# Kernel tuning notes

Measured on AMD Instinct MI355X. Metric: run time of the kernel, lower is better.

## Reference

```python
import jax, jax.numpy as jnp
import numpy as np

NUM_CLASSES = 12
C_SMOOTH = 5.0  # the `c` constant in compute_weights(distances, 5)


def setup_inputs() -> dict:
    key = jax.random.key(0)
    k1, k2 = jax.random.split(key)
    features = jax.random.normal(k1, (128, 512, 32, 32), dtype=jnp.float32)
    labels = jax.random.randint(k2, (128,), 0, NUM_CLASSES)
    return {"features": features, "labels": labels}


def _prototype_generation(features, labels, num_classes):
    # features: [b, c, h, w]; labels: [b] int
    b = features.shape[0]
    flat = features.reshape(b, -1)  # [b, d], d = c*h*w
    sq = jnp.sum(flat * flat, axis=1)  # [b]
    d2 = sq[:, None] + sq[None, :] - 2.0 * (flat @ flat.T)  # [b, b]
    d2 = jnp.maximum(d2, 0.0)
    # grad-safe sqrt: diagonal (and identical pairs) get dist 0 with grad 0,
    # matching torch.norm's subgradient at 0
    pos = d2 > 0
    dist = jnp.where(pos, jnp.sqrt(jnp.where(pos, d2, 1.0)), 0.0)  # [b, b]
    # sum of distances to same-label samples (includes self, dist 0)
    same = (labels[:, None] == labels[None, :]).astype(flat.dtype)  # [b, b]
    dsum = jnp.sum(dist * same, axis=1)  # [b]
    # compute_weights(distance_sum, 5) = 1 / (sqrt(ds^2 + 25) + 1e-12)
    w = 1.0 / (jnp.sqrt(dsum * dsum + C_SMOOTH * C_SMOOTH) + 1e-12)
    w = w / (jnp.sum(w) + 1e-12)  # normalized sample weights [b]
    # label-grouped weighted scatter-sum -> [num_classes, c, h, w]
    weighted = features * w[:, None, None, None]
    return jax.ops.segment_sum(weighted, labels, num_segments=num_classes)


def reference(features, labels):
    return _prototype_generation(features, labels, NUM_CLASSES)
```

## Files before the change

### kernel.cpp

```cpp
#include <hip/hip_runtime.h>
#include <math.h>

#define D_FEAT 524288
#define NSAMP  128
#define NCLS   12
#define BK     256
#define KPB    2048
#define NB     256
#define D4     131072

typedef __bf16 bf16x8 __attribute__((ext_vector_type(8)));
typedef float  f32x16 __attribute__((ext_vector_type(16)));

__device__ __forceinline__ unsigned pack_bf16(float a, float b) {
  unsigned ua = __float_as_uint(a); ua += 0x7fffu + ((ua >> 16) & 1u);
  unsigned ub = __float_as_uint(b); ub += 0x7fffu + ((ub >> 16) & 1u);
  return (ua >> 16) | (ub & 0xffff0000u);
}

__global__ __launch_bounds__(512, 2) void gram_k(const float* __restrict__ f,
                                                 float* __restrict__ gram,
                                                 float* __restrict__ partial,
                                                 int atomic_mode) {
  __shared__ __align__(16) unsigned char lds[BK * NSAMP * 2];
  const int t    = threadIdx.x;
  const int b    = blockIdx.x;
  const int wave = t >> 6;
  const int lane = t & 63;
  const int sl   = lane & 31;
  const int hi   = lane >> 5;
  const int Ra   = (wave >> 2) * 64;
  const int Ca   = (wave & 3) * 32;
  const int kq   = lane;
  const size_t k0 = (size_t)b * KPB;

  f32x16 acc0, acc1;
#pragma unroll
  for (int i = 0; i < 16; ++i) { acc0[i] = 0.f; acc1[i] = 0.f; }

  const int wg      = kq >> 1;
  const int halfsel = kq & 1;

  float4 pf[16];
#pragma unroll
  for (int i = 0; i < 16; ++i) {
    const int s = i * 8 + wave;
    pf[i] = *(const float4*)(f + (size_t)s * D_FEAT + k0 + kq * 4);
  }
#pragma unroll
  for (int i = 0; i < 16; ++i) {
    const int s = i * 8 + wave;
    uint2 p; p.x = pack_bf16(pf[i].x, pf[i].y); p.y = pack_bf16(pf[i].z, pf[i].w);
    *(uint2*)(lds + (size_t)(wg * NSAMP + (s ^ (wg & 7))) * 16 + halfsel * 8) = p;
  }

  for (int sli = 0; sli < KPB / BK; ++sli) {
    __syncthreads();
    if (sli < KPB / BK - 1) {
      const size_t kb = k0 + (size_t)(sli + 1) * BK;
#pragma unroll
      for (int i = 0; i < 16; ++i) {
        const int s = i * 8 + wave;
        pf[i] = *(const float4*)(f + (size_t)s * D_FEAT + kb + kq * 4);
      }
    }
#pragma unroll
    for (int t16 = 0; t16 < 16; ++t16) {
      const int g = 2 * t16 + hi, gx = g & 7;
      const unsigned char* base = lds + g * (NSAMP * 16);
      bf16x8 a0 = *(const bf16x8*)(base + (((Ra      + sl) ^ gx) << 4));
      bf16x8 a1 = *(const bf16x8*)(base + (((Ra + 32 + sl) ^ gx) << 4));
      bf16x8 b0 = *(const bf16x8*)(base + (((Ca      + sl) ^ gx) << 4));
      acc0 = __builtin_amdgcn_mfma_f32_32x32x16_bf16(a0, b0, acc0, 0, 0, 0);
      acc1 = __builtin_amdgcn_mfma_f32_32x32x16_bf16(a1, b0, acc1, 0, 0, 0);
    }
    __syncthreads();
    if (sli < KPB / BK - 1) {
#pragma unroll
      for (int i = 0; i < 16; ++i) {
        const int s = i * 8 + wave;
        uint2 p; p.x = pack_bf16(pf[i].x, pf[i].y); p.y = pack_bf16(pf[i].z, pf[i].w);
        *(uint2*)(lds + (size_t)(wg * NSAMP + (s ^ (wg & 7))) * 16 + halfsel * 8) = p;
      }
    }
  }

  if (atomic_mode) {
#pragma unroll
    for (int r = 0; r < 16; ++r) {
      const int row0 = Ra + 4 * hi + (r & 3) + 8 * (r >> 2);
      atomicAdd(gram + row0 * NSAMP + Ca + sl, acc0[r]);
      atomicAdd(gram + (row0 + 32) * NSAMP + Ca + sl, acc1[r]);
    }
  } else {
    float* p = partial + (size_t)b * (NSAMP * NSAMP);
#pragma unroll
    for (int r = 0; r < 16; ++r) {
      const int row0 = Ra + 4 * hi + (r & 3) + 8 * (r >> 2);
      p[row0 * NSAMP + Ca + sl]        = acc0[r];
      p[(row0 + 32) * NSAMP + Ca + sl] = acc1[r];
    }
  }
}

__global__ __launch_bounds__(256) void reduce_k(const float* __restrict__ partial,
                                                float* __restrict__ gram) {
  const int idx = blockIdx.x * 256 + threadIdx.x;
  float s = 0.f;
#pragma unroll 8
  for (int b = 0; b < NB; ++b) s += partial[(size_t)b * (NSAMP * NSAMP) + idx];
  gram[idx] = s;
}

__global__ void weights_k(const float* __restrict__ gram, const int* __restrict__ labels,
                          float* __restrict__ w_out, int* __restrict__ order_out,
                          int* __restrict__ off_out) {
  __shared__ float sq[NSAMP];
  __shared__ int   lab[NSAMP];
  __shared__ float wv[NSAMP];
  __shared__ float wsum_s;
  __shared__ int   cnt[NCLS];
  __shared__ int   off[NCLS + 1];
  const int t = threadIdx.x;
  lab[t] = labels[t];
  sq[t]  = gram[t * NSAMP + t];
  if (t < NCLS) cnt[t] = 0;
  __syncthreads();
  const int   myl = lab[t];
  const float st  = sq[t];
  float dsum = 0.f;
  for (int j = 0; j < NSAMP; ++j) {
    if (j != t && lab[j] == myl) {
      float d2 = st + sq[j] - 2.f * gram[t * NSAMP + j];
      if (d2 > 0.f) dsum += sqrtf(d2);
    }
  }
  const float wt = 1.f / (sqrtf(dsum * dsum + 25.f) + 1e-12f);
  wv[t] = wt;
  atomicAdd(&cnt[myl], 1);
  __syncthreads();
  if (t == 0) {
    float s = 0.f;
    for (int j = 0; j < NSAMP; ++j) s += wv[j];
    wsum_s = s;
    off[0] = 0;
    for (int c = 0; c < NCLS; ++c) off[c + 1] = off[c] + cnt[c];
  }
  __syncthreads();
  int rank = 0;
  for (int j = 0; j < t; ++j) rank += (lab[j] == myl) ? 1 : 0;
  const int pos  = off[myl] + rank;
  order_out[pos] = t;
  w_out[pos]     = wt / (wsum_s + 1e-12f);
  if (t <= NCLS) off_out[t] = off[t];
}

__global__ __launch_bounds__(256) void scatter_k(const float* __restrict__ f,
                                                 const float* __restrict__ w,
                                                 const int* __restrict__ order,
                                                 const int* __restrict__ off,
                                                 float* __restrict__ out) {
  __shared__ float w_l[NSAMP];
  __shared__ int   ord_l[NSAMP];
  __shared__ int   off_l[NCLS + 1];
  const int t = threadIdx.x;
  if (t < NSAMP) { w_l[t] = w[t]; ord_l[t] = order[t]; }
  if (t <= NCLS) off_l[t] = off[t];
  __syncthreads();
  const size_t d4 = (size_t)blockIdx.x * 256 + t;
  const float4* f4 = (const float4*)f;
  float4* o4 = (float4*)out;
  for (int c = 0; c < NCLS; ++c) {
    float4 acc = make_float4(0.f, 0.f, 0.f, 0.f);
    const int e = off_l[c + 1];
#pragma unroll 4
    for (int j = off_l[c]; j < e; ++j) {
      const float  wj = w_l[j];
      const float4 v  = f4[(size_t)ord_l[j] * D4 + d4];
      acc.x += wj * v.x; acc.y += wj * v.y; acc.z += wj * v.z; acc.w += wj * v.w;
    }
    o4[(size_t)c * D4 + d4] = acc;
  }
}

extern "C" void kernel_launch(void* const* d_in, const int* in_sizes, int n_in,
                              void* d_out, int out_size, void* d_ws, size_t ws_size,
                              hipStream_t stream) {
  const float* f      = (const float*)d_in[0];
  const int*   labels = (const int*)d_in[1];
  float* out  = (float*)d_out;
  float* ws_f = (float*)d_ws;

  float* gram     = ws_f;
  float* w_sorted = ws_f + 16384;
  int*   order    = (int*)(ws_f + 16384 + 128);
  int*   clsoff   = (int*)(ws_f + 16384 + 256);
  float* partial  = ws_f + 32768;

  const size_t need = (size_t)32768 * 4 + (size_t)NB * NSAMP * NSAMP * 4;
  const int atomic_mode = (ws_size < need) ? 1 : 0;

  if (atomic_mode) hipMemsetAsync(gram, 0, NSAMP * NSAMP * sizeof(float), stream);
  gram_k<<<NB, 512, 0, stream>>>(f, gram, partial, atomic_mode);
  if (!atomic_mode) reduce_k<<<64, 256, 0, stream>>>(partial, gram);
  weights_k<<<1, NSAMP, 0, stream>>>(gram, labels, w_sorted, order, clsoff);
  scatter_k<<<D4 / 256, 256, 0, stream>>>(f, w_sorted, order, clsoff, out);
}
```

Baseline: 480.7 us.

## Double gram blocks, split reduction across samples, and parallelize scatter over classes

The gram kernel now uses a half-size K slice per block (512 blocks, BK 128) with higher occupancy hints and a two-samples-per-wave load mapping. The partial reduction splits the block-sum across four thread groups with an LDS combine, giving 256 blocks instead of 64. The scatter kernel gets one block per class per chunk instead of looping over all classes in one block, which spreads the work over many more blocks. The costs are a partial buffer twice as large and more reduction traffic.

```diff
diff --git a/kernel.cpp b/kernel.cpp
--- a/kernel.cpp
+++ b/kernel.cpp
@@ -4,9 +4,9 @@
 #define D_FEAT 524288
 #define NSAMP  128
 #define NCLS   12
-#define BK     256
-#define KPB    2048
-#define NB     256
+#define BK     128
+#define KPB    1024
+#define NB     512
 #define D4     131072
 
 typedef __bf16 bf16x8 __attribute__((ext_vector_type(8)));
@@ -18,7 +18,7 @@
   return (ua >> 16) | (ub & 0xffff0000u);
 }
 
-__global__ __launch_bounds__(512, 2) void gram_k(const float* __restrict__ f,
+__global__ __launch_bounds__(512, 4) void gram_k(const float* __restrict__ f,
                                                  float* __restrict__ gram,
                                                  float* __restrict__ partial,
                                                  int atomic_mode) {
@@ -31,25 +31,25 @@
   const int hi   = lane >> 5;
   const int Ra   = (wave >> 2) * 64;
   const int Ca   = (wave & 3) * 32;
-  const int kq   = lane;
+  const int q    = lane & 31;
   const size_t k0 = (size_t)b * KPB;
 
   f32x16 acc0, acc1;
 #pragma unroll
   for (int i = 0; i < 16; ++i) { acc0[i] = 0.f; acc1[i] = 0.f; }
 
-  const int wg      = kq >> 1;
-  const int halfsel = kq & 1;
-
-  float4 pf[16];
-#pragma unroll
-  for (int i = 0; i < 16; ++i) {
-    const int s = i * 8 + wave;
-    pf[i] = *(const float4*)(f + (size_t)s * D_FEAT + k0 + kq * 4);
-  }
-#pragma unroll
-  for (int i = 0; i < 16; ++i) {
-    const int s = i * 8 + wave;
+  const int wg      = q >> 1;
+  const int halfsel = q & 1;
+
+  float4 pf[8];
+#pragma unroll
+  for (int i = 0; i < 8; ++i) {
+    const int s = i * 16 + wave * 2 + hi;
+    pf[i] = *(const float4*)(f + (size_t)s * D_FEAT + k0 + q * 4);
+  }
+#pragma unroll
+  for (int i = 0; i < 8; ++i) {
+    const int s = i * 16 + wave * 2 + hi;
     uint2 p; p.x = pack_bf16(pf[i].x, pf[i].y); p.y = pack_bf16(pf[i].z, pf[i].w);
     *(uint2*)(lds + (size_t)(wg * NSAMP + (s ^ (wg & 7))) * 16 + halfsel * 8) = p;
   }
@@ -59,14 +59,14 @@
     if (sli < KPB / BK - 1) {
       const size_t kb = k0 + (size_t)(sli + 1) * BK;
 #pragma unroll
-      for (int i = 0; i < 16; ++i) {
-        const int s = i * 8 + wave;
-        pf[i] = *(const float4*)(f + (size_t)s * D_FEAT + kb + kq * 4);
+      for (int i = 0; i < 8; ++i) {
+        const int s = i * 16 + wave * 2 + hi;
+        pf[i] = *(const float4*)(f + (size_t)s * D_FEAT + kb + q * 4);
       }
     }
 #pragma unroll
-    for (int t16 = 0; t16 < 16; ++t16) {
-      const int g = 2 * t16 + hi, gx = g & 7;
+    for (int step = 0; step < BK / 16; ++step) {
+      const int g = 2 * step + hi, gx = g & 7;
       const unsigned char* base = lds + g * (NSAMP * 16);
       bf16x8 a0 = *(const bf16x8*)(base + (((Ra      + sl) ^ gx) << 4));
       bf16x8 a1 = *(const bf16x8*)(base + (((Ra + 32 + sl) ^ gx) << 4));
@@ -77,8 +77,8 @@
     __syncthreads();
     if (sli < KPB / BK - 1) {
 #pragma unroll
-      for (int i = 0; i < 16; ++i) {
-        const int s = i * 8 + wave;
+      for (int i = 0; i < 8; ++i) {
+        const int s = i * 16 + wave * 2 + hi;
         uint2 p; p.x = pack_bf16(pf[i].x, pf[i].y); p.y = pack_bf16(pf[i].z, pf[i].w);
         *(uint2*)(lds + (size_t)(wg * NSAMP + (s ^ (wg & 7))) * 16 + halfsel * 8) = p;
       }
@@ -105,11 +105,17 @@
 
 __global__ __launch_bounds__(256) void reduce_k(const float* __restrict__ partial,
                                                 float* __restrict__ gram) {
-  const int idx = blockIdx.x * 256 + threadIdx.x;
+  __shared__ float red[256];
+  const int t  = threadIdx.x;
+  const int o  = blockIdx.x * 64 + (t & 63);
+  const int bs = t >> 6;
   float s = 0.f;
 #pragma unroll 8
-  for (int b = 0; b < NB; ++b) s += partial[(size_t)b * (NSAMP * NSAMP) + idx];
-  gram[idx] = s;
+  for (int b = bs * (NB / 4); b < (bs + 1) * (NB / 4); ++b)
+    s += partial[(size_t)b * (NSAMP * NSAMP) + o];
+  red[t] = s;
+  __syncthreads();
+  if (t < 64) gram[o] = red[t] + red[t + 64] + red[t + 128] + red[t + 192];
 }
 
 __global__ void weights_k(const float* __restrict__ gram, const int* __restrict__ labels,
@@ -162,25 +168,25 @@
                                                  float* __restrict__ out) {
   __shared__ float w_l[NSAMP];
   __shared__ int   ord_l[NSAMP];
-  __shared__ int   off_l[NCLS + 1];
-  const int t = threadIdx.x;
+  __shared__ int   jr[2];
+  const int t  = threadIdx.x;
+  const int c  = blockIdx.x >> 9;
+  const int cb = blockIdx.x & 511;
   if (t < NSAMP) { w_l[t] = w[t]; ord_l[t] = order[t]; }
-  if (t <= NCLS) off_l[t] = off[t];
-  __syncthreads();
-  const size_t d4 = (size_t)blockIdx.x * 256 + t;
+  if (t < 2) jr[t] = off[c + t];
+  __syncthreads();
+  const int j0 = jr[0], j1 = jr[1];
+  const size_t d4 = (size_t)cb * 256 + t;
   const float4* f4 = (const float4*)f;
   float4* o4 = (float4*)out;
-  for (int c = 0; c < NCLS; ++c) {
-    float4 acc = make_float4(0.f, 0.f, 0.f, 0.f);
-    const int e = off_l[c + 1];
+  float4 acc = make_float4(0.f, 0.f, 0.f, 0.f);
 #pragma unroll 4
-    for (int j = off_l[c]; j < e; ++j) {
-      const float  wj = w_l[j];
-      const float4 v  = f4[(size_t)ord_l[j] * D4 + d4];
-      acc.x += wj * v.x; acc.y += wj * v.y; acc.z += wj * v.z; acc.w += wj * v.w;
-    }
-    o4[(size_t)c * D4 + d4] = acc;
-  }
+  for (int j = j0; j < j1; ++j) {
+    const float  wj = w_l[j];
+    const float4 v  = f4[(size_t)ord_l[j] * D4 + d4];
+    acc.x += wj * v.x; acc.y += wj * v.y; acc.z += wj * v.z; acc.w += wj * v.w;
+  }
+  o4[(size_t)c * D4 + d4] = acc;
 }
 
 extern "C" void kernel_launch(void* const* d_in, const int* in_sizes, int n_in,
@@ -202,7 +208,7 @@
 
   if (atomic_mode) hipMemsetAsync(gram, 0, NSAMP * NSAMP * sizeof(float), stream);
   gram_k<<<NB, 512, 0, stream>>>(f, gram, partial, atomic_mode);
-  if (!atomic_mode) reduce_k<<<64, 256, 0, stream>>>(partial, gram);
+  if (!atomic_mode) reduce_k<<<NSAMP * NSAMP / 64, 256, 0, stream>>>(partial, gram);
   weights_k<<<1, NSAMP, 0, stream>>>(gram, labels, w_sorted, order, clsoff);
-  scatter_k<<<D4 / 256, 256, 0, stream>>>(f, w_sorted, order, clsoff, out);
-}
+  scatter_k<<<NCLS * 512, 256, 0, stream>>>(f, w_sorted, order, clsoff, out);
+}
```

New measurement: 486.7 us. Within noise of the previous version (+1.2%).
